# Performance work log

Measured on AMD Instinct MI355X. Metric: run time of the kernel, lower is better.

## Reference

```python
import jax, jax.numpy as jnp
import numpy as np

N = 100000      # nodes
E = 1280000     # edges
D_IN = 64       # in_channels
D_OUT = 64      # out_channels
D_EDGE = 16     # edge_dim
NEG_SLOPE = 0.01  # torch F.leaky_relu default


def setup_inputs() -> dict:
    key = jax.random.key(0)
    ks = jax.random.split(key, 8)
    x = jax.random.normal(ks[0], (N, D_IN), dtype=jnp.float32)
    edge_attr = jax.random.normal(ks[1], (E, D_EDGE), dtype=jnp.float32)
    src = jax.random.randint(ks[2], (E,), 0, N, dtype=jnp.int32)
    dst = jax.random.randint(ks[3], (E,), 0, N, dtype=jnp.int32)
    # parameters (xavier-like scale)
    W1 = jax.random.normal(ks[4], (D_OUT, D_IN + D_EDGE), dtype=jnp.float32) * (2.0 / (D_OUT + D_IN + D_EDGE)) ** 0.5
    W2 = jax.random.normal(ks[5], (D_OUT, D_IN), dtype=jnp.float32) * (2.0 / (D_OUT + D_IN)) ** 0.5
    attn = jax.random.normal(ks[6], (D_OUT + D_IN,), dtype=jnp.float32) * (2.0 / (1 + D_OUT + D_IN)) ** 0.5
    bias = jnp.zeros((D_OUT,), dtype=jnp.float32)
    return {"x": x, "edge_attr": edge_attr, "src": src, "dst": dst,
            "W1": W1, "W2": W2, "attn": attn, "bias": bias}


def reference(x, edge_attr, src, dst, W1, W2, attn, bias):
    # node transform: lin2
    x_t = x @ W2.T                                    # [N, D_OUT]
    # per-edge gathers
    x_l = x[src]                                      # [E, D_IN]
    x_r = x[dst]                                      # [E, D_IN]
    # lin1 on [x_l || edge_attr]
    f_srt = jnp.concatenate([x_l, edge_attr], axis=-1) @ W1.T   # [E, D_OUT]
    e = jax.nn.leaky_relu(jnp.concatenate([f_srt, x_r], axis=-1), NEG_SLOPE)  # [E, D_OUT+D_IN]
    logits = e @ attn                                 # [E]
    # edge_softmax over destination-node segments
    seg_max = jax.ops.segment_max(logits, dst, num_segments=N)
    seg_max = jnp.where(jnp.isfinite(seg_max), seg_max, 0.0)
    expd = jnp.exp(logits - seg_max[dst])             # [E]
    denom = jax.ops.segment_sum(expd, dst, num_segments=N)
    alpha = expd / denom[dst]                         # [E]  (dropout p=0 -> identity)
    # scatter-sum aggregation: sum_e alpha_e * x_t[src_e] into dst
    msgs = x_t[src] * alpha[:, None]                  # [E, D_OUT]
    h = jax.ops.segment_sum(msgs, dst, num_segments=N)
    return h + bias
```

## Files before the change

### kernel.cpp

```cpp
#include <hip/hip_runtime.h>

#define D 64
#define D_EDGE 16
#define NEG 0.01f

typedef unsigned int  uint32;
typedef unsigned short ushort16;

__device__ __forceinline__ float leaky(float v) { return fmaxf(v, NEG * v); }

__device__ __forceinline__ ushort16 f2bf(float f) {
    uint32 b = __float_as_uint(f);
    uint32 r = b + 0x7fffu + ((b >> 16) & 1u);
    return (ushort16)(r >> 16);
}
__device__ __forceinline__ float bf2f(ushort16 u) {
    return __uint_as_float(((uint32)u) << 16);
}
__device__ __forceinline__ float bf_lo(uint32 w) { return __uint_as_float(w << 16); }
__device__ __forceinline__ float bf_hi(uint32 w) { return __uint_as_float(w & 0xffff0000u); }

__global__ __launch_bounds__(256) void node_kernel(
    const float* __restrict__ x, const float* __restrict__ W1,
    const float* __restrict__ W2,
    ushort16* __restrict__ Abf, ushort16* __restrict__ xtb, int N_)
{
    __shared__ float xs[64][68];
    uint32* sA = (uint32*)&xs[0][0];
    uint32* sX = sA + 64 * 33;

    const int tid = threadIdx.x;
    const int b0  = blockIdx.x * 64;

    for (int idx = tid; idx < 64 * 16; idx += 256) {
        const int rr = idx >> 4, cc = idx & 15;
        float4 v = make_float4(0.f, 0.f, 0.f, 0.f);
        if (b0 + rr < N_) v = ((const float4*)(x + (size_t)(b0 + rr) * D))[cc];
        *(float4*)&xs[rr][cc * 4] = v;
    }
    __syncthreads();

    const int lane = tid & 63;
    const int q    = __builtin_amdgcn_readfirstlane(tid >> 6);

    float4 xr[16];
#pragma unroll
    for (int i = 0; i < 16; i++) xr[i] = *(const float4*)&xs[lane][4 * i];
    __syncthreads();

    float a_prev = 0.f, b_prev = 0.f;
#pragma unroll
    for (int kk = 0; kk < 16; kk++) {
        const int k = q * 16 + kk;
        const float4* w2r = (const float4*)(W2 + (size_t)k * 64);
        const float4* w1r = (const float4*)(W1 + (size_t)k * 80);
        float a = 0.f, b = 0.f;
#pragma unroll
        for (int j = 0; j < 16; j++) {
            float4 w = w2r[j];
            a += xr[j].x * w.x + xr[j].y * w.y + xr[j].z * w.z + xr[j].w * w.w;
            float4 u = w1r[j];
            b += xr[j].x * u.x + xr[j].y * u.y + xr[j].z * u.z + xr[j].w * u.w;
        }
        if (kk & 1) {
            const int pr = k >> 1;
            sX[lane * 33 + pr] = (uint32)f2bf(a_prev) | ((uint32)f2bf(a) << 16);
            sA[lane * 33 + pr] = (uint32)f2bf(b_prev) | ((uint32)f2bf(b) << 16);
        } else {
            a_prev = a; b_prev = b;
        }
    }
    __syncthreads();

    uint32* Au = (uint32*)Abf;
    uint32* Xu = (uint32*)xtb;
    const size_t gbase = (size_t)b0 * 32;
    for (int base = tid * 4; base < 2048; base += 1024) {
        const int nn = base >> 5, cc = base & 31;
        if (b0 + nn < N_) {
            const uint32* ra = sA + nn * 33 + cc;
            const uint32* rx = sX + nn * 33 + cc;
            uint4 va = make_uint4(ra[0], ra[1], ra[2], ra[3]);
            uint4 vx = make_uint4(rx[0], rx[1], rx[2], rx[3]);
            *(uint4*)(Au + gbase + base) = va;
            *(uint4*)(Xu + gbase + base) = vx;
        }
    }
}

__global__ __launch_bounds__(256) void hist_kernel(
    const int* __restrict__ dst, int* __restrict__ cnt, int E_)
{
    int i = blockIdx.x * 256 + threadIdx.x;
    if (i < E_) atomicAdd(cnt + dst[i], 1);
}

__global__ __launch_bounds__(256) void scan1(
    const int* __restrict__ cnt, int* __restrict__ part, int N_)
{
    __shared__ int sm[256];
    const int b = blockIdx.x, t = threadIdx.x;
    const int i0 = b * 1024 + t * 4;
    int s = 0;
    if (i0     < N_) s += cnt[i0];
    if (i0 + 1 < N_) s += cnt[i0 + 1];
    if (i0 + 2 < N_) s += cnt[i0 + 2];
    if (i0 + 3 < N_) s += cnt[i0 + 3];
    sm[t] = s; __syncthreads();
    for (int off = 128; off > 0; off >>= 1) {
        if (t < off) sm[t] += sm[t + off];
        __syncthreads();
    }
    if (t == 0) part[b] = sm[0];
}

__global__ __launch_bounds__(256) void scan2(int* __restrict__ part, int nb)
{
    __shared__ int sm[256];
    const int t = threadIdx.x;
    int v = (t < nb) ? part[t] : 0;
    sm[t] = v; __syncthreads();
    for (int off = 1; off < 256; off <<= 1) {
        int a = (t >= off) ? sm[t - off] : 0;
        __syncthreads();
        sm[t] += a;
        __syncthreads();
    }
    if (t < nb) part[t] = sm[t] - v;
}

__global__ __launch_bounds__(256) void scan3(
    const int* __restrict__ cnt, const int* __restrict__ part,
    int* __restrict__ rowst, int N_)
{
    __shared__ int sm[256];
    const int b = blockIdx.x, t = threadIdx.x;
    const int i0 = b * 1024 + t * 4;
    int c0 = 0, c1 = 0, c2 = 0, c3 = 0;
    if (i0     < N_) c0 = cnt[i0];
    if (i0 + 1 < N_) c1 = cnt[i0 + 1];
    if (i0 + 2 < N_) c2 = cnt[i0 + 2];
    if (i0 + 3 < N_) c3 = cnt[i0 + 3];
    const int s = c0 + c1 + c2 + c3;
    sm[t] = s; __syncthreads();
    for (int off = 1; off < 256; off <<= 1) {
        int a = (t >= off) ? sm[t - off] : 0;
        __syncthreads();
        sm[t] += a;
        __syncthreads();
    }
    const int base = part[b] + (sm[t] - s);
    if (i0     < N_) rowst[i0]     = base;
    if (i0 + 1 < N_) rowst[i0 + 1] = base + c0;
    if (i0 + 2 < N_) rowst[i0 + 2] = base + c0 + c1;
    if (i0 + 3 < N_) rowst[i0 + 3] = base + c0 + c1 + c2;
}

__global__ __launch_bounds__(256) void edge_kernel(
    const float* __restrict__ edge_attr, const int* __restrict__ src,
    const int* __restrict__ dst, const float* __restrict__ W1,
    const float* __restrict__ attn, const ushort16* __restrict__ Abf,
    int* __restrict__ rowpos, int2* __restrict__ SP, int E_)
{
    const int e = blockIdx.x * 256 + threadIdx.x;
    if (e >= E_) return;

    const int s = src[e];
    const int d = dst[e];

    uint32 Ad[32];
    {
        const uint4* Ap = (const uint4*)(Abf + (size_t)s * D);
#pragma unroll
        for (int i = 0; i < 8; i++) *(uint4*)(Ad + 4 * i) = Ap[i];
    }
    float Ef[16];
    {
        const float4* Ep = (const float4*)(edge_attr + (size_t)e * D_EDGE);
#pragma unroll
        for (int i = 0; i < 4; i++) *(float4*)(Ef + 4 * i) = Ep[i];
    }

    float v = 0.f;
#pragma unroll
    for (int j = 0; j < 32; ++j) {
        const float4* w0 = (const float4*)(W1 + (2 * j) * 80 + 64);
        const float4* w1 = (const float4*)(W1 + (2 * j + 1) * 80 + 64);
        float4 p0 = w0[0], p1 = w0[1], p2 = w0[2], p3 = w0[3];
        float4 q0 = w1[0], q1 = w1[1], q2 = w1[2], q3 = w1[3];

        float g0 = bf_lo(Ad[j]);
        float g1 = bf_hi(Ad[j]);

        g0 = fmaf(Ef[ 0], p0.x, g0); g1 = fmaf(Ef[ 0], q0.x, g1);
        g0 = fmaf(Ef[ 1], p0.y, g0); g1 = fmaf(Ef[ 1], q0.y, g1);
        g0 = fmaf(Ef[ 2], p0.z, g0); g1 = fmaf(Ef[ 2], q0.z, g1);
        g0 = fmaf(Ef[ 3], p0.w, g0); g1 = fmaf(Ef[ 3], q0.w, g1);
        g0 = fmaf(Ef[ 4], p1.x, g0); g1 = fmaf(Ef[ 4], q1.x, g1);
        g0 = fmaf(Ef[ 5], p1.y, g0); g1 = fmaf(Ef[ 5], q1.y, g1);
        g0 = fmaf(Ef[ 6], p1.z, g0); g1 = fmaf(Ef[ 6], q1.z, g1);
        g0 = fmaf(Ef[ 7], p1.w, g0); g1 = fmaf(Ef[ 7], q1.w, g1);
        g0 = fmaf(Ef[ 8], p2.x, g0); g1 = fmaf(Ef[ 8], q2.x, g1);
        g0 = fmaf(Ef[ 9], p2.y, g0); g1 = fmaf(Ef[ 9], q2.y, g1);
        g0 = fmaf(Ef[10], p2.z, g0); g1 = fmaf(Ef[10], q2.z, g1);
        g0 = fmaf(Ef[11], p2.w, g0); g1 = fmaf(Ef[11], q2.w, g1);
        g0 = fmaf(Ef[12], p3.x, g0); g1 = fmaf(Ef[12], q3.x, g1);
        g0 = fmaf(Ef[13], p3.y, g0); g1 = fmaf(Ef[13], q3.y, g1);
        g0 = fmaf(Ef[14], p3.z, g0); g1 = fmaf(Ef[14], q3.z, g1);
        g0 = fmaf(Ef[15], p3.w, g0); g1 = fmaf(Ef[15], q3.w, g1);

        v = fmaf(leaky(g0), attn[2 * j],     v);
        v = fmaf(leaky(g1), attn[2 * j + 1], v);
    }

    const float p = __expf(v);
    const int pos = atomicAdd(rowpos + d, 1);
    SP[pos] = make_int2(s, __float_as_int(p));
}

__global__ __launch_bounds__(256) void agg_kernel(
    const ushort16* __restrict__ xtb, const int2* __restrict__ SP,
    const int* __restrict__ rowend, const float* __restrict__ bias,
    float* __restrict__ out, int N_)
{
    const int n    = blockIdx.x * 4 + (threadIdx.x >> 6);
    const int lane = threadIdx.x & 63;
    if (n >= N_) return;
    const int half = lane >> 5;
    const int c    = lane & 31;

    const int end   = rowend[n];
    const int start = n ? rowend[n - 1] : 0;
    const uint32* X = (const uint32*)xtb;

    float accx = 0.f, accy = 0.f, den = 0.f;
    int i = start;
    for (; i + 7 < end; i += 8) {
        int2 A0 = SP[i+0], A1 = SP[i+1], A2 = SP[i+2], A3 = SP[i+3];
        int2 A4 = SP[i+4], A5 = SP[i+5], A6 = SP[i+6], A7 = SP[i+7];
        int   r0 = half ? A1.x : A0.x;  float p0 = __int_as_float(half ? A1.y : A0.y);
        int   r1 = half ? A3.x : A2.x;  float p1 = __int_as_float(half ? A3.y : A2.y);
        int   r2 = half ? A5.x : A4.x;  float p2 = __int_as_float(half ? A5.y : A4.y);
        int   r3 = half ? A7.x : A6.x;  float p3 = __int_as_float(half ? A7.y : A6.y);
        uint32 u0 = X[(size_t)r0 * 32 + c];
        uint32 u1 = X[(size_t)r1 * 32 + c];
        uint32 u2 = X[(size_t)r2 * 32 + c];
        uint32 u3 = X[(size_t)r3 * 32 + c];
        accx = fmaf(p0, bf_lo(u0), accx); accy = fmaf(p0, bf_hi(u0), accy);
        accx = fmaf(p1, bf_lo(u1), accx); accy = fmaf(p1, bf_hi(u1), accy);
        accx = fmaf(p2, bf_lo(u2), accx); accy = fmaf(p2, bf_hi(u2), accy);
        accx = fmaf(p3, bf_lo(u3), accx); accy = fmaf(p3, bf_hi(u3), accy);
        den += (p0 + p1) + (p2 + p3);
    }
    for (; i < end; i++) {
        int2 a = SP[i];
        if (half == 0) {
            float p = __int_as_float(a.y);
            uint32 u = X[(size_t)a.x * 32 + c];
            accx = fmaf(p, bf_lo(u), accx);
            accy = fmaf(p, bf_hi(u), accy);
            den += p;
        }
    }
    accx += __shfl_xor(accx, 32, 64);
    accy += __shfl_xor(accy, 32, 64);
    den  += __shfl_xor(den,  32, 64);

    if (half == 0) {
        const float sc = den > 0.f ? 1.f / den : 0.f;
        const float2 bb = *(const float2*)(bias + 2 * c);
        float2 o;
        o.x = fmaf(accx, sc, bb.x);
        o.y = fmaf(accy, sc, bb.y);
        *(float2*)(out + (size_t)n * D + 2 * c) = o;
    }
}

extern "C" void kernel_launch(void* const* d_in, const int* in_sizes, int n_in,
                              void* d_out, int out_size, void* d_ws, size_t ws_size,
                              hipStream_t stream)
{
    const float* x         = (const float*)d_in[0];
    const float* edge_attr = (const float*)d_in[1];
    const int*   src       = (const int*)d_in[2];
    const int*   dst       = (const int*)d_in[3];
    const float* W1        = (const float*)d_in[4];
    const float* W2        = (const float*)d_in[5];
    const float* attn      = (const float*)d_in[6];
    const float* bias      = (const float*)d_in[7];
    float* out = (float*)d_out;

    const int N_ = in_sizes[0] / D;
    const int E_ = in_sizes[2];

    char* w = (char*)d_ws;
    ushort16* Abf  = (ushort16*)w;  w += (size_t)N_ * D * sizeof(ushort16);
    ushort16* xtb  = (ushort16*)w;  w += (size_t)N_ * D * sizeof(ushort16);
    int2*     SP   = (int2*)w;      w += (size_t)E_ * sizeof(int2);
    int*      rowst= (int*)w;       w += (size_t)N_ * sizeof(int);
    int*      cnt  = (int*)w;       w += (size_t)N_ * sizeof(int);
    int*      part = (int*)w;

    hipMemsetAsync(cnt, 0, (size_t)N_ * sizeof(int), stream);

    const int NB1 = (N_ + 1023) / 1024;

    hist_kernel<<<(E_ + 255) / 256, 256, 0, stream>>>(dst, cnt, E_);
    scan1<<<NB1, 256, 0, stream>>>(cnt, part, N_);
    scan2<<<1, 256, 0, stream>>>(part, NB1);
    scan3<<<NB1, 256, 0, stream>>>(cnt, part, rowst, N_);

    node_kernel<<<(N_ + 63) / 64, 256, 0, stream>>>(x, W1, W2, Abf, xtb, N_);

    edge_kernel<<<(E_ + 255) / 256, 256, 0, stream>>>(edge_attr, src, dst, W1,
                                                      attn, Abf, rowst, SP, E_);

    agg_kernel<<<(N_ + 3) / 4, 256, 0, stream>>>(xtb, SP, rowst, bias, out, N_);
}
```

Measured before the change: 414.2 us.

## Sort edges by source via extra counting pass before edge logit kernel

Adds a source-node histogram next to the destination histogram and scans both together, folding the scan2 kernel into scan3. A new scatter kernel packs each edge's attributes to bf16 together with src and dst into 48-byte records placed in source-sorted order, so the edge kernel's gathers of per-node Abf rows become mostly sequential and cache-friendly. This costs an extra pass that reads edge_attr and writes about 61 MB of records, plus a second set of atomics, and rounds edge attributes to bf16. It falls back to the original edge kernel when the workspace is too small.

```diff
diff --git a/kernel.cpp b/kernel.cpp
--- a/kernel.cpp
+++ b/kernel.cpp
@@ -19,6 +19,9 @@
 }
 __device__ __forceinline__ float bf_lo(uint32 w) { return __uint_as_float(w << 16); }
 __device__ __forceinline__ float bf_hi(uint32 w) { return __uint_as_float(w & 0xffff0000u); }
+__device__ __forceinline__ uint32 pk(float a, float b) {
+    return (uint32)f2bf(a) | ((uint32)f2bf(b) << 16);
+}
 
 __global__ __launch_bounds__(256) void node_kernel(
     const float* __restrict__ x, const float* __restrict__ W1,
@@ -64,8 +67,8 @@
         }
         if (kk & 1) {
             const int pr = k >> 1;
-            sX[lane * 33 + pr] = (uint32)f2bf(a_prev) | ((uint32)f2bf(a) << 16);
-            sA[lane * 33 + pr] = (uint32)f2bf(b_prev) | ((uint32)f2bf(b) << 16);
+            sX[lane * 33 + pr] = pk(a_prev, a);
+            sA[lane * 33 + pr] = pk(b_prev, b);
         } else {
             a_prev = a; b_prev = b;
         }
@@ -80,32 +83,34 @@
         if (b0 + nn < N_) {
             const uint32* ra = sA + nn * 33 + cc;
             const uint32* rx = sX + nn * 33 + cc;
-            uint4 va = make_uint4(ra[0], ra[1], ra[2], ra[3]);
-            uint4 vx = make_uint4(rx[0], rx[1], rx[2], rx[3]);
-            *(uint4*)(Au + gbase + base) = va;
-            *(uint4*)(Xu + gbase + base) = vx;
+            *(uint4*)(Au + gbase + base) = make_uint4(ra[0], ra[1], ra[2], ra[3]);
+            *(uint4*)(Xu + gbase + base) = make_uint4(rx[0], rx[1], rx[2], rx[3]);
         }
     }
 }
 
-__global__ __launch_bounds__(256) void hist_kernel(
-    const int* __restrict__ dst, int* __restrict__ cnt, int E_)
+__global__ __launch_bounds__(256) void hist2_kernel(
+    const int* __restrict__ dst, const int* __restrict__ src,
+    int* __restrict__ cnt2, int N_, int E_)
 {
     int i = blockIdx.x * 256 + threadIdx.x;
-    if (i < E_) atomicAdd(cnt + dst[i], 1);
+    if (i < E_) {
+        atomicAdd(cnt2 + dst[i], 1);
+        atomicAdd(cnt2 + N_ + src[i], 1);
+    }
 }
 
 __global__ __launch_bounds__(256) void scan1(
-    const int* __restrict__ cnt, int* __restrict__ part, int N_)
+    const int* __restrict__ cnt, int* __restrict__ part, int N2_)
 {
     __shared__ int sm[256];
     const int b = blockIdx.x, t = threadIdx.x;
     const int i0 = b * 1024 + t * 4;
     int s = 0;
-    if (i0     < N_) s += cnt[i0];
-    if (i0 + 1 < N_) s += cnt[i0 + 1];
-    if (i0 + 2 < N_) s += cnt[i0 + 2];
-    if (i0 + 3 < N_) s += cnt[i0 + 3];
+    if (i0     < N2_) s += cnt[i0];
+    if (i0 + 1 < N2_) s += cnt[i0 + 1];
+    if (i0 + 2 < N2_) s += cnt[i0 + 2];
+    if (i0 + 3 < N2_) s += cnt[i0 + 3];
     sm[t] = s; __syncthreads();
     for (int off = 128; off > 0; off >>= 1) {
         if (t < off) sm[t] += sm[t + off];
@@ -114,33 +119,30 @@
     if (t == 0) part[b] = sm[0];
 }
 
-__global__ __launch_bounds__(256) void scan2(int* __restrict__ part, int nb)
-{
-    __shared__ int sm[256];
-    const int t = threadIdx.x;
-    int v = (t < nb) ? part[t] : 0;
-    sm[t] = v; __syncthreads();
-    for (int off = 1; off < 256; off <<= 1) {
-        int a = (t >= off) ? sm[t - off] : 0;
-        __syncthreads();
-        sm[t] += a;
-        __syncthreads();
-    }
-    if (t < nb) part[t] = sm[t] - v;
-}
-
 __global__ __launch_bounds__(256) void scan3(
     const int* __restrict__ cnt, const int* __restrict__ part,
-    int* __restrict__ rowst, int N_)
-{
+    int* __restrict__ rowst, int N2_, int nb)
+{
+    __shared__ int sp[256];
     __shared__ int sm[256];
     const int b = blockIdx.x, t = threadIdx.x;
+
+    sp[t] = (t < nb) ? part[t] : 0;
+    __syncthreads();
+    for (int off = 1; off < 256; off <<= 1) {
+        int a = (t >= off) ? sp[t - off] : 0;
+        __syncthreads();
+        sp[t] += a;
+        __syncthreads();
+    }
+    const int pbase = (b > 0) ? sp[b - 1] : 0;
+
     const int i0 = b * 1024 + t * 4;
     int c0 = 0, c1 = 0, c2 = 0, c3 = 0;
-    if (i0     < N_) c0 = cnt[i0];
-    if (i0 + 1 < N_) c1 = cnt[i0 + 1];
-    if (i0 + 2 < N_) c2 = cnt[i0 + 2];
-    if (i0 + 3 < N_) c3 = cnt[i0 + 3];
+    if (i0     < N2_) c0 = cnt[i0];
+    if (i0 + 1 < N2_) c1 = cnt[i0 + 1];
+    if (i0 + 2 < N2_) c2 = cnt[i0 + 2];
+    if (i0 + 3 < N2_) c3 = cnt[i0 + 3];
     const int s = c0 + c1 + c2 + c3;
     sm[t] = s; __syncthreads();
     for (int off = 1; off < 256; off <<= 1) {
@@ -149,36 +151,61 @@
         sm[t] += a;
         __syncthreads();
     }
-    const int base = part[b] + (sm[t] - s);
-    if (i0     < N_) rowst[i0]     = base;
-    if (i0 + 1 < N_) rowst[i0 + 1] = base + c0;
-    if (i0 + 2 < N_) rowst[i0 + 2] = base + c0 + c1;
-    if (i0 + 3 < N_) rowst[i0 + 3] = base + c0 + c1 + c2;
-}
-
-__global__ __launch_bounds__(256) void edge_kernel(
+    const int base = pbase + (sm[t] - s);
+    if (i0     < N2_) rowst[i0]     = base;
+    if (i0 + 1 < N2_) rowst[i0 + 1] = base + c0;
+    if (i0 + 2 < N2_) rowst[i0 + 2] = base + c0 + c1;
+    if (i0 + 3 < N2_) rowst[i0 + 3] = base + c0 + c1 + c2;
+}
+
+__global__ __launch_bounds__(256) void scatter_kernel(
     const float* __restrict__ edge_attr, const int* __restrict__ src,
-    const int* __restrict__ dst, const float* __restrict__ W1,
+    const int* __restrict__ dst, int* __restrict__ srowpos,
+    uint4* __restrict__ REC, int E_)
+{
+    const int e = blockIdx.x * 256 + threadIdx.x;
+    if (e >= E_) return;
+    const int s = src[e];
+    const int d = dst[e];
+    const float4* ea = (const float4*)(edge_attr + (size_t)e * D_EDGE);
+    float4 q0 = ea[0], q1 = ea[1], q2 = ea[2], q3 = ea[3];
+
+    const int pos = atomicAdd(srowpos + s, 1) - E_;
+    uint4* R = REC + (size_t)pos * 3;
+    R[0] = make_uint4(pk(q0.x, q0.y), pk(q0.z, q0.w), pk(q1.x, q1.y), pk(q1.z, q1.w));
+    R[1] = make_uint4(pk(q2.x, q2.y), pk(q2.z, q2.w), pk(q3.x, q3.y), pk(q3.z, q3.w));
+    R[2] = make_uint4((uint32)s, (uint32)d, 0u, 0u);
+}
+
+__global__ __launch_bounds__(256) void edge_kernel_sorted(
+    const uint4* __restrict__ REC, const float* __restrict__ W1,
     const float* __restrict__ attn, const ushort16* __restrict__ Abf,
     int* __restrict__ rowpos, int2* __restrict__ SP, int E_)
 {
-    const int e = blockIdx.x * 256 + threadIdx.x;
-    if (e >= E_) return;
-
-    const int s = src[e];
-    const int d = dst[e];
+    const int i = blockIdx.x * 256 + threadIdx.x;
+    if (i >= E_) return;
+
+    uint4 r0 = REC[(size_t)i * 3 + 0];
+    uint4 r1 = REC[(size_t)i * 3 + 1];
+    uint4 r2 = REC[(size_t)i * 3 + 2];
+    const int s = (int)r2.x;
+    const int d = (int)r2.y;
+
+    float Ef[16];
+    Ef[ 0] = bf_lo(r0.x); Ef[ 1] = bf_hi(r0.x);
+    Ef[ 2] = bf_lo(r0.y); Ef[ 3] = bf_hi(r0.y);
+    Ef[ 4] = bf_lo(r0.z); Ef[ 5] = bf_hi(r0.z);
+    Ef[ 6] = bf_lo(r0.w); Ef[ 7] = bf_hi(r0.w);
+    Ef[ 8] = bf_lo(r1.x); Ef[ 9] = bf_hi(r1.x);
+    Ef[10] = bf_lo(r1.y); Ef[11] = bf_hi(r1.y);
+    Ef[12] = bf_lo(r1.z); Ef[13] = bf_hi(r1.z);
+    Ef[14] = bf_lo(r1.w); Ef[15] = bf_hi(r1.w);
 
     uint32 Ad[32];
     {
         const uint4* Ap = (const uint4*)(Abf + (size_t)s * D);
 #pragma unroll
-        for (int i = 0; i < 8; i++) *(uint4*)(Ad + 4 * i) = Ap[i];
-    }
-    float Ef[16];
-    {
-        const float4* Ep = (const float4*)(edge_attr + (size_t)e * D_EDGE);
-#pragma unroll
-        for (int i = 0; i < 4; i++) *(float4*)(Ef + 4 * i) = Ep[i];
+        for (int t = 0; t < 8; t++) *(uint4*)(Ad + 4 * t) = Ap[t];
     }
 
     float v = 0.f;
@@ -209,6 +236,64 @@
         g0 = fmaf(Ef[14], p3.z, g0); g1 = fmaf(Ef[14], q3.z, g1);
         g0 = fmaf(Ef[15], p3.w, g0); g1 = fmaf(Ef[15], q3.w, g1);
 
+        v = fmaf(leaky(g0), attn[2 * j],     v);
+        v = fmaf(leaky(g1), attn[2 * j + 1], v);
+    }
+
+    const float p = __expf(v);
+    const int pos = atomicAdd(rowpos + d, 1);
+    SP[pos] = make_int2(s, __float_as_int(p));
+}
+
+__global__ __launch_bounds__(256) void edge_kernel_orig(
+    const float* __restrict__ edge_attr, const int* __restrict__ src,
+    const int* __restrict__ dst, const float* __restrict__ W1,
+    const float* __restrict__ attn, const ushort16* __restrict__ Abf,
+    int* __restrict__ rowpos, int2* __restrict__ SP, int E_)
+{
+    const int e = blockIdx.x * 256 + threadIdx.x;
+    if (e >= E_) return;
+    const int s = src[e];
+    const int d = dst[e];
+
+    uint32 Ad[32];
+    {
+        const uint4* Ap = (const uint4*)(Abf + (size_t)s * D);
+#pragma unroll
+        for (int t = 0; t < 8; t++) *(uint4*)(Ad + 4 * t) = Ap[t];
+    }
+    float Ef[16];
+    {
+        const float4* Ep = (const float4*)(edge_attr + (size_t)e * D_EDGE);
+#pragma unroll
+        for (int t = 0; t < 4; t++) *(float4*)(Ef + 4 * t) = Ep[t];
+    }
+
+    float v = 0.f;
+#pragma unroll
+    for (int j = 0; j < 32; ++j) {
+        const float4* w0 = (const float4*)(W1 + (2 * j) * 80 + 64);
+        const float4* w1 = (const float4*)(W1 + (2 * j + 1) * 80 + 64);
+        float4 p0 = w0[0], p1 = w0[1], p2 = w0[2], p3 = w0[3];
+        float4 q0 = w1[0], q1 = w1[1], q2 = w1[2], q3 = w1[3];
+        float g0 = bf_lo(Ad[j]);
+        float g1 = bf_hi(Ad[j]);
+        g0 = fmaf(Ef[ 0], p0.x, g0); g1 = fmaf(Ef[ 0], q0.x, g1);
+        g0 = fmaf(Ef[ 1], p0.y, g0); g1 = fmaf(Ef[ 1], q0.y, g1);
+        g0 = fmaf(Ef[ 2], p0.z, g0); g1 = fmaf(Ef[ 2], q0.z, g1);
+        g0 = fmaf(Ef[ 3], p0.w, g0); g1 = fmaf(Ef[ 3], q0.w, g1);
+        g0 = fmaf(Ef[ 4], p1.x, g0); g1 = fmaf(Ef[ 4], q1.x, g1);
+        g0 = fmaf(Ef[ 5], p1.y, g0); g1 = fmaf(Ef[ 5], q1.y, g1);
+        g0 = fmaf(Ef[ 6], p1.z, g0); g1 = fmaf(Ef[ 6], q1.z, g1);
+        g0 = fmaf(Ef[ 7], p1.w, g0); g1 = fmaf(Ef[ 7], q1.w, g1);
+        g0 = fmaf(Ef[ 8], p2.x, g0); g1 = fmaf(Ef[ 8], q2.x, g1);
+        g0 = fmaf(Ef[ 9], p2.y, g0); g1 = fmaf(Ef[ 9], q2.y, g1);
+        g0 = fmaf(Ef[10], p2.z, g0); g1 = fmaf(Ef[10], q2.z, g1);
+        g0 = fmaf(Ef[11], p2.w, g0); g1 = fmaf(Ef[11], q2.w, g1);
+        g0 = fmaf(Ef[12], p3.x, g0); g1 = fmaf(Ef[12], q3.x, g1);
+        g0 = fmaf(Ef[13], p3.y, g0); g1 = fmaf(Ef[13], q3.y, g1);
+        g0 = fmaf(Ef[14], p3.z, g0); g1 = fmaf(Ef[14], q3.z, g1);
+        g0 = fmaf(Ef[15], p3.w, g0); g1 = fmaf(Ef[15], q3.w, g1);
         v = fmaf(leaky(g0), attn[2 * j],     v);
         v = fmaf(leaky(g1), attn[2 * j + 1], v);
     }
@@ -292,28 +377,41 @@
 
     const int N_ = in_sizes[0] / D;
     const int E_ = in_sizes[2];
+    const int N2 = 2 * N_;
 
     char* w = (char*)d_ws;
     ushort16* Abf  = (ushort16*)w;  w += (size_t)N_ * D * sizeof(ushort16);
     ushort16* xtb  = (ushort16*)w;  w += (size_t)N_ * D * sizeof(ushort16);
     int2*     SP   = (int2*)w;      w += (size_t)E_ * sizeof(int2);
-    int*      rowst= (int*)w;       w += (size_t)N_ * sizeof(int);
-    int*      cnt  = (int*)w;       w += (size_t)N_ * sizeof(int);
-    int*      part = (int*)w;
-
-    hipMemsetAsync(cnt, 0, (size_t)N_ * sizeof(int), stream);
-
-    const int NB1 = (N_ + 1023) / 1024;
-
-    hist_kernel<<<(E_ + 255) / 256, 256, 0, stream>>>(dst, cnt, E_);
-    scan1<<<NB1, 256, 0, stream>>>(cnt, part, N_);
-    scan2<<<1, 256, 0, stream>>>(part, NB1);
-    scan3<<<NB1, 256, 0, stream>>>(cnt, part, rowst, N_);
+    uint4*    REC  = (uint4*)w;
+    const size_t rec_bytes = (size_t)E_ * 48;
+    const size_t fixed_tail = (size_t)N2 * 4 * 2 + 1024;
+    const size_t base_used  = (size_t)((char*)REC - (char*)d_ws);
+    const bool   sorted = (base_used + rec_bytes + fixed_tail) <= ws_size;
+    if (sorted) w += rec_bytes;
+    int* rowst2 = (int*)w;          w += (size_t)N2 * sizeof(int);
+    int* cnt2   = (int*)w;          w += (size_t)N2 * sizeof(int);
+    int* part   = (int*)w;
+
+    hipMemsetAsync(cnt2, 0, (size_t)N2 * sizeof(int), stream);
+
+    const int NB = (N2 + 1023) / 1024;
+
+    hist2_kernel<<<(E_ + 255) / 256, 256, 0, stream>>>(dst, src, cnt2, N_, E_);
+    scan1<<<NB, 256, 0, stream>>>(cnt2, part, N2);
+    scan3<<<NB, 256, 0, stream>>>(cnt2, part, rowst2, N2, NB);
 
     node_kernel<<<(N_ + 63) / 64, 256, 0, stream>>>(x, W1, W2, Abf, xtb, N_);
 
-    edge_kernel<<<(E_ + 255) / 256, 256, 0, stream>>>(edge_attr, src, dst, W1,
-                                                      attn, Abf, rowst, SP, E_);
-
-    agg_kernel<<<(N_ + 3) / 4, 256, 0, stream>>>(xtb, SP, rowst, bias, out, N_);
-}
+    if (sorted) {
+        scatter_kernel<<<(E_ + 255) / 256, 256, 0, stream>>>(
+            edge_attr, src, dst, rowst2 + N_, REC, E_);
+        edge_kernel_sorted<<<(E_ + 255) / 256, 256, 0, stream>>>(
+            REC, W1, attn, Abf, rowst2, SP, E_);
+    } else {
+        edge_kernel_orig<<<(E_ + 255) / 256, 256, 0, stream>>>(
+            edge_attr, src, dst, W1, attn, Abf, rowst2, SP, E_);
+    }
+
+    agg_kernel<<<(N_ + 3) / 4, 256, 0, stream>>>(xtb, SP, rowst2, bias, out, N_);
+}
```

Result: slower. 504.0 us (+21.7%).
